# Optimization experiments

Hardware: AMD Instinct MI355X
Metric: run time of the kernel (lower is better)

Reference implementation:

```python
import jax, jax.numpy as jnp
import numpy as np

T = 2_000_000  # timesteps


def setup_inputs() -> dict:
    key = jax.random.key(0)
    u = jax.random.normal(key, (T, 2), dtype=jnp.float32) * 10.0  # external forces per step
    x0 = jnp.zeros((4,), dtype=jnp.float32)  # [z1, v1, z2, v2]
    c = jnp.array([10.0, 10.0, 10.0], dtype=jnp.float32)   # trainable damping c1,c2,c3
    m = jnp.array([20.0, 10.0], dtype=jnp.float32)          # masses m1,m2 (frozen)
    k = jnp.array([2.0e3, 1.0e3, 5.0e3], dtype=jnp.float32) # stiffness k1,k2,k3 (frozen)
    dt = jnp.float32(0.002)
    return {"u": u, "x0": x0, "c": c, "m": m, "k": k, "dt": dt}


def reference(u, x0, c, m, k, dt):
    c1, c2, c3 = c[0], c[1], c[2]
    m1, m2 = m[0], m[1]
    k1, k2, k3 = k[0], k[1], k[2]

    def deriv(x, ut):
        # x = [z1, v1, z2, v2]; returns dx/dt = [v1, a1, v2, a2]
        z1, v1, z2, v2 = x[0], x[1], x[2], x[3]
        a1 = (ut[0] - (c1 + c2) * v1 + c2 * v2 - (k1 + k2) * z1 + k2 * z2) / m1
        a2 = (ut[1] - (c3 + c2) * v2 + c2 * v1 - (k3 + k2) * z2 + k2 * z1) / m2
        return jnp.stack([v1, a1, v2, a2])

    half = dt * 0.5

    def step(x, ut):
        s1 = deriv(x, ut)
        s2 = deriv(x + half * s1, ut)
        s3 = deriv(x + half * s2, ut)
        s4 = deriv(x + dt * s3, ut)
        xn = x + (dt / 6.0) * (s1 + 2.0 * s2 + 2.0 * s3 + s4)
        y = jnp.stack([xn[0], xn[2]])  # positions z1, z2 (matches cell output)
        return xn, y

    _, ys = jax.lax.scan(step, x0, u)
    return ys  # [T, 2]
```

## Files before the change

kernel.cpp:

```cpp
#include <hip/hip_runtime.h>

#define BLK 256
#define LS  16
#define SPB (BLK*LS)
#define STR (LS+1)

#define WC_M   0
#define WC_N   16
#define WC_SK  24
#define WC_GK  152
#define WC_TOT 296
#define WS_AGG 320

#define STEP4(Mx,Nx, s0,s1,s2,s3, ux,uy, n0,n1,n2,n3)                                              \
  n0 = fmaf(Mx[0],s0,  fmaf(Mx[1],s1,  fmaf(Mx[2],s2,  fmaf(Mx[3],s3,  fmaf(Nx[0],ux, Nx[1]*uy))))); \
  n1 = fmaf(Mx[4],s0,  fmaf(Mx[5],s1,  fmaf(Mx[6],s2,  fmaf(Mx[7],s3,  fmaf(Nx[2],ux, Nx[3]*uy))))); \
  n2 = fmaf(Mx[8],s0,  fmaf(Mx[9],s1,  fmaf(Mx[10],s2, fmaf(Mx[11],s3, fmaf(Nx[4],ux, Nx[5]*uy))))); \
  n3 = fmaf(Mx[12],s0, fmaf(Mx[13],s1, fmaf(Mx[14],s2, fmaf(Mx[15],s3, fmaf(Nx[6],ux, Nx[7]*uy)))));

__device__ __forceinline__ float4 aff_apply(const float* Mx, float4 l, float4 c) {
  float4 r;
  r.x = fmaf(Mx[0],l.x,  fmaf(Mx[1],l.y,  fmaf(Mx[2],l.z,  fmaf(Mx[3],l.w,  c.x))));
  r.y = fmaf(Mx[4],l.x,  fmaf(Mx[5],l.y,  fmaf(Mx[6],l.z,  fmaf(Mx[7],l.w,  c.y))));
  r.z = fmaf(Mx[8],l.x,  fmaf(Mx[9],l.y,  fmaf(Mx[10],l.z, fmaf(Mx[11],l.w, c.z))));
  r.w = fmaf(Mx[12],l.x, fmaf(Mx[13],l.y, fmaf(Mx[14],l.z, fmaf(Mx[15],l.w, c.w))));
  return r;
}

__device__ __forceinline__ float4 matvec(const float* Mx, float4 v) {
  return aff_apply(Mx, v, make_float4(0.f, 0.f, 0.f, 0.f));
}

__device__ __forceinline__ float4 shfl_up4(float4 v, int d) {
  return make_float4(__shfl_up(v.x, d, 64), __shfl_up(v.y, d, 64),
                     __shfl_up(v.z, d, 64), __shfl_up(v.w, d, 64));
}

__device__ __forceinline__ double mm_el(double x, double y, int i, int j) {
  double s = 0.0;
  #pragma unroll
  for (int l = 0; l < 4; ++l)
    s = fma(__shfl(x, 4*i + l, 64), __shfl(y, 4*l + j, 64), s);
  return s;
}

__device__ __forceinline__ void wave_setup(const float* __restrict__ cin,
                                           const float* __restrict__ min_,
                                           const float* __restrict__ kin,
                                           const float* __restrict__ dtin,
                                           float* C, int lane, bool wantGK) {
  double c1 = cin[0], c2 = cin[1], c3 = cin[2];
  double m1 = min_[0], m2 = min_[1];
  double k1 = kin[0], k2 = kin[1], k3 = kin[2];
  double h  = dtin[0];
  const int i = (lane >> 2) & 3, j = lane & 3;

  double a;
  if (i == 0)      a = (j == 1) ? 1.0 : 0.0;
  else if (i == 2) a = (j == 3) ? 1.0 : 0.0;
  else if (i == 1) a = (j==0) ? -(k1+k2)/m1 : (j==1) ? -(c1+c2)/m1
                     : (j==2) ?  k2/m1      :  c2/m1;
  else             a = (j==0) ?  k2/m2      : (j==1) ?  c2/m2
                     : (j==2) ? -(k3+k2)/m2 : -(c3+c2)/m2;

  const double id = (i == j) ? 1.0 : 0.0;
  double q  = id + (h/4.0)*a;
  double t  = mm_el(a, q,  i, j);
  double r  = id + (h/3.0)*t;
  t         = mm_el(a, r,  i, j);
  double s_ = id + (h/2.0)*t;
  t         = mm_el(a, s_, i, j);
  double m  = id + h*t;
  if (lane < 16) C[WC_M + lane] = (float)m;

  {
    int e = lane & 7, ii = e >> 1, jp = e & 1, col = jp ? 3 : 1;
    double sv = __shfl(s_, 4*ii + col, 64);
    double nv = h * sv / (jp ? m2 : m1);
    if (lane < 8) C[WC_N + lane] = (float)nv;
  }

  double p = m;
  #pragma unroll
  for (int rr = 0; rr < 4; ++rr) p = mm_el(p, p, i, j);
  if (lane < 16) C[WC_SK + lane] = (float)p;
  #pragma unroll
  for (int k = 1; k < 8; ++k) {
    p = mm_el(p, p, i, j);
    if (lane < 16) C[WC_SK + 16*k + lane] = (float)p;
  }
  if (wantGK) {
    p = mm_el(p, p, i, j);
    if (lane < 16) C[WC_GK + lane] = (float)p;
    #pragma unroll
    for (int k = 1; k < 9; ++k) {
      p = mm_el(p, p, i, j);
      if (lane < 16) C[WC_GK + 16*k + lane] = (float)p;
    }
  }
}

__device__ __forceinline__ float4 wave_scan(const float* SK, float4 b, int lane) {
  float4 cur = b;
  #pragma unroll
  for (int k = 0; k < 6; ++k) {
    int off = 1 << k;
    float4 l  = shfl_up4(cur, off);
    float4 nv = aff_apply(&SK[16*k], l, cur);
    if (lane >= off) cur = nv;
  }
  return cur;
}

__device__ __forceinline__ float4 cross_wave_excl(const float* SK, const float4* Wagg, int w) {
  float4 E = make_float4(0.f, 0.f, 0.f, 0.f);
  if (w > 0) {
    E = Wagg[0];
    for (int q = 1; q < w; ++q) E = aff_apply(&SK[16*6], E, Wagg[q]);
  }
  return E;
}

__launch_bounds__(BLK)
__global__ void k_pass1(const float4* __restrict__ u4,
                        const float* __restrict__ cc, const float* __restrict__ mmp,
                        const float* __restrict__ kp, const float* __restrict__ dtp,
                        float* __restrict__ wsc, float4* __restrict__ agg, int T2) {
  __shared__ float  uxp[BLK*STR];
  __shared__ float  uyp[BLK*STR];
  __shared__ float  C[WC_TOT];
  __shared__ float4 Wagg[4];
  const int tid   = threadIdx.x;
  const int bid   = blockIdx.x;
  const int lane  = tid & 63, w = tid >> 6;
  const int base2 = bid * SPB;

  if (tid < 64) wave_setup(cc, mmp, kp, dtp, C, tid, bid == 0);

  #pragma unroll
  for (int kk = 0; kk < SPB/2/BLK; ++kk) {
    int idx4 = tid + kk*BLK;
    int s0 = 2*idx4;
    float4 v = make_float4(0.f, 0.f, 0.f, 0.f);
    if (base2 + s0 < T2) v = u4[(base2 >> 1) + idx4];
    int t0 = s0 >> 4, j0 = s0 & 15;
    int t1 = (s0+1) >> 4, j1 = (s0+1) & 15;
    uxp[t0*STR + j0] = v.x;  uyp[t0*STR + j0] = v.y;
    uxp[t1*STR + j1] = v.z;  uyp[t1*STR + j1] = v.w;
  }
  __syncthreads();

  if (bid == 0)
    for (int i = tid; i < WC_TOT; i += BLK) wsc[i] = C[i];

  float Mm[16], Nn[8];
  #pragma unroll
  for (int i = 0; i < 16; ++i) Mm[i] = C[WC_M+i];
  #pragma unroll
  for (int i = 0; i < 8;  ++i) Nn[i] = C[WC_N+i];
  const float* SK = &C[WC_SK];

  float b0 = 0.f, b1 = 0.f, b2 = 0.f, b3 = 0.f;
  #pragma unroll
  for (int j = 0; j < LS; ++j) {
    float ux = uxp[tid*STR + j], uy = uyp[tid*STR + j];
    float n0, n1, n2, n3;
    STEP4(Mm, Nn, b0, b1, b2, b3, ux, uy, n0, n1, n2, n3);
    b0 = n0; b1 = n1; b2 = n2; b3 = n3;
  }

  float4 incl = wave_scan(SK, make_float4(b0, b1, b2, b3), lane);
  if (lane == 63) Wagg[w] = incl;
  __syncthreads();

  if (tid == BLK-1) {
    float4 E = cross_wave_excl(SK, Wagg, 3);
    float4 t_ = matvec(&SK[16*6], E);
    agg[bid] = make_float4(incl.x + t_.x, incl.y + t_.y, incl.z + t_.z, incl.w + t_.w);
  }
}

__launch_bounds__(BLK)
__global__ void k_pass3(const float4* __restrict__ u4,
                        const float* __restrict__ wsc,
                        const float4* __restrict__ agg,
                        const float* __restrict__ x0in, float4* __restrict__ out4,
                        int T2, int nblk) {
  __shared__ float  uxp[BLK*STR];
  __shared__ float  uyp[BLK*STR];
  __shared__ float4 MA[512];
  __shared__ float4 MB[512];
  __shared__ float  C[WC_TOT];
  __shared__ float4 Wagg[4];
  const int tid   = threadIdx.x;
  const int bid   = blockIdx.x;
  const int lane  = tid & 63, w = tid >> 6;
  const int base2 = bid * SPB;

  for (int i = tid; i < WC_TOT; i += BLK) C[i] = wsc[i];

  #pragma unroll
  for (int kk = 0; kk < SPB/2/BLK; ++kk) {
    int idx4 = tid + kk*BLK;
    int s0 = 2*idx4;
    float4 v = make_float4(0.f, 0.f, 0.f, 0.f);
    if (base2 + s0 < T2) v = u4[(base2 >> 1) + idx4];
    int t0 = s0 >> 4, j0 = s0 & 15;
    int t1 = (s0+1) >> 4, j1 = (s0+1) & 15;
    uxp[t0*STR + j0] = v.x;  uyp[t0*STR + j0] = v.y;
    uxp[t1*STR + j1] = v.z;  uyp[t1*STR + j1] = v.w;
  }

  const int n = nblk + 1;
  #pragma unroll
  for (int j = 0; j < 2; ++j) {
    int i = tid + BLK*j;
    if (i < n) MA[i] = (i == 0) ? make_float4(x0in[0], x0in[1], x0in[2], x0in[3])
                                : agg[i-1];
  }
  __syncthreads();

  float Mm[16], Nn[8];
  #pragma unroll
  for (int i = 0; i < 16; ++i) Mm[i] = C[WC_M+i];
  #pragma unroll
  for (int i = 0; i < 8;  ++i) Nn[i] = C[WC_N+i];
  const float* SK = &C[WC_SK];
  const float* GK = &C[WC_GK];

  float b0 = 0.f, b1 = 0.f, b2 = 0.f, b3 = 0.f;
  #pragma unroll
  for (int j = 0; j < LS; ++j) {
    float ux = uxp[tid*STR + j], uy = uyp[tid*STR + j];
    float n0, n1, n2, n3;
    STEP4(Mm, Nn, b0, b1, b2, b3, ux, uy, n0, n1, n2, n3);
    b0 = n0; b1 = n1; b2 = n2; b3 = n3;
  }
  float4 incl = wave_scan(SK, make_float4(b0, b1, b2, b3), lane);
  if (lane == 63) Wagg[w] = incl;

  float4* Aa = MA; float4* Bb = MB;
  for (int k = 0; k < 9; ++k) {
    int off = 1 << k;
    if (off >= n) break;
    #pragma unroll
    for (int j = 0; j < 2; ++j) {
      int i = tid + BLK*j;
      if (i < n) {
        float4 v = Aa[i];
        if (i >= off) v = aff_apply(&GK[16*k], Aa[i-off], v);
        Bb[i] = v;
      }
    }
    __syncthreads();
    float4* t = Aa; Aa = Bb; Bb = t;
  }

  float4 Xbs = Aa[bid];

  float4 E  = cross_wave_excl(SK, Wagg, w);
  float4 Xw = Xbs;
  if (w & 1) Xw = matvec(&SK[16*6], Xw);
  if (w & 2) Xw = matvec(&SK[16*7], Xw);
  Xw = make_float4(Xw.x + E.x, Xw.y + E.y, Xw.z + E.z, Xw.w + E.w);

  float4 ex = shfl_up4(incl, 1);
  if (lane == 0) ex = make_float4(0.f, 0.f, 0.f, 0.f);
  float4 v = Xw;
  #pragma unroll
  for (int k = 0; k < 6; ++k)
    if (lane & (1 << k)) v = matvec(&SK[16*k], v);
  float x0 = v.x + ex.x, x1 = v.y + ex.y, x2 = v.z + ex.z, x3 = v.w + ex.w;

  #pragma unroll
  for (int j = 0; j < LS; ++j) {
    float ux = uxp[tid*STR + j], uy = uyp[tid*STR + j];
    float n0, n1, n2, n3;
    STEP4(Mm, Nn, x0, x1, x2, x3, ux, uy, n0, n1, n2, n3);
    x0 = n0; x1 = n1; x2 = n2; x3 = n3;
    uxp[tid*STR + j] = x0;
    uyp[tid*STR + j] = x2;
  }
  __syncthreads();

  #pragma unroll
  for (int kk = 0; kk < SPB/2/BLK; ++kk) {
    int idx4 = tid + kk*BLK;
    int s0 = 2*idx4;
    if (base2 + s0 < T2) {
      int t0 = s0 >> 4, j0 = s0 & 15;
      int t1 = (s0+1) >> 4, j1 = (s0+1) & 15;
      out4[(base2 >> 1) + idx4] = make_float4(uxp[t0*STR + j0], uyp[t0*STR + j0],
                                              uxp[t1*STR + j1], uyp[t1*STR + j1]);
    }
  }
}

extern "C" void kernel_launch(void* const* d_in, const int* in_sizes, int n_in,
                              void* d_out, int out_size, void* d_ws, size_t ws_size,
                              hipStream_t stream) {
  const float* u   = (const float*)d_in[0];
  const float* x0  = (const float*)d_in[1];
  const float* cc  = (const float*)d_in[2];
  const float* mm  = (const float*)d_in[3];
  const float* kk  = (const float*)d_in[4];
  const float* dt  = (const float*)d_in[5];

  const int T2   = in_sizes[0] / 2;
  const int nblk = (T2 + SPB - 1) / SPB;

  float*  ws  = (float*)d_ws;
  float4* agg = (float4*)(ws + WS_AGG);

  k_pass1<<<nblk, BLK, 0, stream>>>((const float4*)u, cc, mm, kk, dt, ws, agg, T2);
  k_pass3<<<nblk, BLK, 0, stream>>>((const float4*)u, ws, agg, x0,
                                    (float4*)d_out, T2, nblk);
}
```

Baseline: 95.91 us.

## Fuse two scan passes into one kernel with a grid-wide atomic barrier

Merges the aggregate pass and the final pass into a single kernel. Each block computes its local aggregate, publishes it, then spins on a global atomic counter until every block has arrived. This removes the second kernel launch and the second global read of u, since the inputs stay resident in shared memory. In exchange every block recomputes the constant matrices, the launch needs a memset of the counter, and correctness depends on all blocks (about 489) being co-resident on the device.

```diff
diff --git a/kernel.cpp b/kernel.cpp
--- a/kernel.cpp
+++ b/kernel.cpp
@@ -10,7 +10,8 @@
 #define WC_SK  24
 #define WC_GK  152
 #define WC_TOT 296
-#define WS_AGG 320
+
+#define WS_BAR_OFF (512*4)
 
 #define STEP4(Mx,Nx, s0,s1,s2,s3, ux,uy, n0,n1,n2,n3)                                              \
   n0 = fmaf(Mx[0],s0,  fmaf(Mx[1],s1,  fmaf(Mx[2],s2,  fmaf(Mx[3],s3,  fmaf(Nx[0],ux, Nx[1]*uy))))); \
@@ -48,7 +49,7 @@
                                            const float* __restrict__ min_,
                                            const float* __restrict__ kin,
                                            const float* __restrict__ dtin,
-                                           float* C, int lane, bool wantGK) {
+                                           float* C, int lane) {
   double c1 = cin[0], c2 = cin[1], c3 = cin[2];
   double m1 = min_[0], m2 = min_[1];
   double k1 = kin[0], k2 = kin[1], k3 = kin[2];
@@ -89,14 +90,12 @@
     p = mm_el(p, p, i, j);
     if (lane < 16) C[WC_SK + 16*k + lane] = (float)p;
   }
-  if (wantGK) {
+  p = mm_el(p, p, i, j);
+  if (lane < 16) C[WC_GK + lane] = (float)p;
+  #pragma unroll
+  for (int k = 1; k < 9; ++k) {
     p = mm_el(p, p, i, j);
-    if (lane < 16) C[WC_GK + lane] = (float)p;
-    #pragma unroll
-    for (int k = 1; k < 9; ++k) {
-      p = mm_el(p, p, i, j);
-      if (lane < 16) C[WC_GK + 16*k + lane] = (float)p;
-    }
+    if (lane < 16) C[WC_GK + 16*k + lane] = (float)p;
   }
 }
 
@@ -121,69 +120,11 @@
   return E;
 }
 
-__launch_bounds__(BLK)
-__global__ void k_pass1(const float4* __restrict__ u4,
+__launch_bounds__(BLK, 2)
+__global__ void k_fused(const float4* __restrict__ u4,
                         const float* __restrict__ cc, const float* __restrict__ mmp,
                         const float* __restrict__ kp, const float* __restrict__ dtp,
-                        float* __restrict__ wsc, float4* __restrict__ agg, int T2) {
-  __shared__ float  uxp[BLK*STR];
-  __shared__ float  uyp[BLK*STR];
-  __shared__ float  C[WC_TOT];
-  __shared__ float4 Wagg[4];
-  const int tid   = threadIdx.x;
-  const int bid   = blockIdx.x;
-  const int lane  = tid & 63, w = tid >> 6;
-  const int base2 = bid * SPB;
-
-  if (tid < 64) wave_setup(cc, mmp, kp, dtp, C, tid, bid == 0);
-
-  #pragma unroll
-  for (int kk = 0; kk < SPB/2/BLK; ++kk) {
-    int idx4 = tid + kk*BLK;
-    int s0 = 2*idx4;
-    float4 v = make_float4(0.f, 0.f, 0.f, 0.f);
-    if (base2 + s0 < T2) v = u4[(base2 >> 1) + idx4];
-    int t0 = s0 >> 4, j0 = s0 & 15;
-    int t1 = (s0+1) >> 4, j1 = (s0+1) & 15;
-    uxp[t0*STR + j0] = v.x;  uyp[t0*STR + j0] = v.y;
-    uxp[t1*STR + j1] = v.z;  uyp[t1*STR + j1] = v.w;
-  }
-  __syncthreads();
-
-  if (bid == 0)
-    for (int i = tid; i < WC_TOT; i += BLK) wsc[i] = C[i];
-
-  float Mm[16], Nn[8];
-  #pragma unroll
-  for (int i = 0; i < 16; ++i) Mm[i] = C[WC_M+i];
-  #pragma unroll
-  for (int i = 0; i < 8;  ++i) Nn[i] = C[WC_N+i];
-  const float* SK = &C[WC_SK];
-
-  float b0 = 0.f, b1 = 0.f, b2 = 0.f, b3 = 0.f;
-  #pragma unroll
-  for (int j = 0; j < LS; ++j) {
-    float ux = uxp[tid*STR + j], uy = uyp[tid*STR + j];
-    float n0, n1, n2, n3;
-    STEP4(Mm, Nn, b0, b1, b2, b3, ux, uy, n0, n1, n2, n3);
-    b0 = n0; b1 = n1; b2 = n2; b3 = n3;
-  }
-
-  float4 incl = wave_scan(SK, make_float4(b0, b1, b2, b3), lane);
-  if (lane == 63) Wagg[w] = incl;
-  __syncthreads();
-
-  if (tid == BLK-1) {
-    float4 E = cross_wave_excl(SK, Wagg, 3);
-    float4 t_ = matvec(&SK[16*6], E);
-    agg[bid] = make_float4(incl.x + t_.x, incl.y + t_.y, incl.z + t_.z, incl.w + t_.w);
-  }
-}
-
-__launch_bounds__(BLK)
-__global__ void k_pass3(const float4* __restrict__ u4,
-                        const float* __restrict__ wsc,
-                        const float4* __restrict__ agg,
+                        float4* __restrict__ agg, unsigned* __restrict__ bar,
                         const float* __restrict__ x0in, float4* __restrict__ out4,
                         int T2, int nblk) {
   __shared__ float  uxp[BLK*STR];
@@ -197,7 +138,7 @@
   const int lane  = tid & 63, w = tid >> 6;
   const int base2 = bid * SPB;
 
-  for (int i = tid; i < WC_TOT; i += BLK) C[i] = wsc[i];
+  if (tid < 64) wave_setup(cc, mmp, kp, dtp, C, tid);
 
   #pragma unroll
   for (int kk = 0; kk < SPB/2/BLK; ++kk) {
@@ -210,14 +151,6 @@
     uxp[t0*STR + j0] = v.x;  uyp[t0*STR + j0] = v.y;
     uxp[t1*STR + j1] = v.z;  uyp[t1*STR + j1] = v.w;
   }
-
-  const int n = nblk + 1;
-  #pragma unroll
-  for (int j = 0; j < 2; ++j) {
-    int i = tid + BLK*j;
-    if (i < n) MA[i] = (i == 0) ? make_float4(x0in[0], x0in[1], x0in[2], x0in[3])
-                                : agg[i-1];
-  }
   __syncthreads();
 
   float Mm[16], Nn[8];
@@ -236,8 +169,32 @@
     STEP4(Mm, Nn, b0, b1, b2, b3, ux, uy, n0, n1, n2, n3);
     b0 = n0; b1 = n1; b2 = n2; b3 = n3;
   }
+
   float4 incl = wave_scan(SK, make_float4(b0, b1, b2, b3), lane);
   if (lane == 63) Wagg[w] = incl;
+  __syncthreads();
+
+  if (tid == BLK-1) {
+    float4 E = cross_wave_excl(SK, Wagg, 3);
+    float4 t_ = matvec(&SK[16*6], E);
+    agg[bid] = make_float4(incl.x + t_.x, incl.y + t_.y, incl.z + t_.z, incl.w + t_.w);
+    __threadfence();
+    __hip_atomic_fetch_add(bar, 1u, __ATOMIC_RELEASE, __HIP_MEMORY_SCOPE_AGENT);
+    while (__hip_atomic_load(bar, __ATOMIC_ACQUIRE, __HIP_MEMORY_SCOPE_AGENT)
+           < (unsigned)nblk)
+      __builtin_amdgcn_s_sleep(2);
+  }
+  __syncthreads();
+  __threadfence();
+
+  const int n = nblk + 1;
+  #pragma unroll
+  for (int j = 0; j < 2; ++j) {
+    int i = tid + BLK*j;
+    if (i < n) MA[i] = (i == 0) ? make_float4(x0in[0], x0in[1], x0in[2], x0in[3])
+                                : agg[i-1];
+  }
+  __syncthreads();
 
   float4* Aa = MA; float4* Bb = MB;
   for (int k = 0; k < 9; ++k) {
@@ -299,20 +256,22 @@
 extern "C" void kernel_launch(void* const* d_in, const int* in_sizes, int n_in,
                               void* d_out, int out_size, void* d_ws, size_t ws_size,
                               hipStream_t stream) {
-  const float* u   = (const float*)d_in[0];
-  const float* x0  = (const float*)d_in[1];
-  const float* cc  = (const float*)d_in[2];
-  const float* mm  = (const float*)d_in[3];
-  const float* kk  = (const float*)d_in[4];
-  const float* dt  = (const float*)d_in[5];
-
-  const int T2   = in_sizes[0] / 2;
-  const int nblk = (T2 + SPB - 1) / SPB;
-
-  float*  ws  = (float*)d_ws;
-  float4* agg = (float4*)(ws + WS_AGG);
-
-  k_pass1<<<nblk, BLK, 0, stream>>>((const float4*)u, cc, mm, kk, dt, ws, agg, T2);
-  k_pass3<<<nblk, BLK, 0, stream>>>((const float4*)u, ws, agg, x0,
+  const float4* u4  = (const float4*)d_in[0];
+  const float*  x0  = (const float*)d_in[1];
+  const float*  cc  = (const float*)d_in[2];
+  const float*  mm  = (const float*)d_in[3];
+  const float*  kk  = (const float*)d_in[4];
+  const float*  dt  = (const float*)d_in[5];
+
+  int T2   = in_sizes[0] / 2;
+  int nblk = (T2 + SPB - 1) / SPB;
+
+  float*    ws  = (float*)d_ws;
+  float4*   agg = (float4*)ws;
+  unsigned* bar = (unsigned*)(ws + WS_BAR_OFF);
+
+  hipMemsetAsync((void*)bar, 0, sizeof(unsigned), stream);
+
+  k_fused<<<nblk, BLK, 0, stream>>>(u4, cc, mm, kk, dt, agg, bar, x0,
                                     (float4*)d_out, T2, nblk);
 }
```

Result: slower. 154.0 us (+60.6%).
